# Kernel tuning notes

Hardware: AMD Instinct MI355X
Metric: run time of the kernel (lower is better)

The kernel has to match this reference:

```python
import jax, jax.numpy as jnp
import numpy as np

B, N, K, CIN, COUT = 2, 8192, 16, 64, 64


def setup_inputs() -> dict:
    key = jax.random.key(0)
    ks = jax.random.split(key, 12)
    w = lambda k, shape: jax.random.normal(k, shape, jnp.float32) * 0.02
    return dict(
        pos=jax.random.normal(ks[0], (B, N, 3), jnp.float32),
        features=jax.random.normal(ks[1], (B, N, CIN), jnp.float32),
        emb_w=w(ks[2], (CIN, COUT)), emb_b=jnp.zeros((COUT,), jnp.float32),
        wq=w(ks[3], (COUT, COUT)), wk=w(ks[4], (COUT, COUT)), wv=w(ks[5], (COUT, COUT)),
        pe_w1=w(ks[6], (3, COUT)), pe_b1=jnp.zeros((COUT,), jnp.float32),
        pe_w2=w(ks[7], (COUT, COUT)), pe_b2=jnp.zeros((COUT,), jnp.float32),
        at_w1=w(ks[8], (COUT, COUT)), at_b1=jnp.zeros((COUT,), jnp.float32),
        at_w2=w(ks[9], (COUT, COUT)), at_b2=jnp.zeros((COUT,), jnp.float32),
        out_w=w(ks[10], (COUT, CIN)), out_b=jnp.zeros((CIN,), jnp.float32),
    )


def _gather(x, idx):
    # x: [B, N, C], idx: [B, N, K] -> [B, N, K, C]
    return jax.vmap(lambda xb, ib: xb[ib])(x, idx)


def reference(pos, features, emb_w, emb_b, wq, wk, wv,
              pe_w1, pe_b1, pe_w2, pe_b2,
              at_w1, at_b1, at_w2, at_b2, out_w, out_b):
    # KNN: squared pairwise distances, take k smallest (includes self)
    sq = jnp.sum(pos * pos, axis=-1)                                  # [B, N]
    d2 = sq[:, :, None] + sq[:, None, :] - 2.0 * jnp.einsum('bnd,bmd->bnm', pos, pos)
    _, knn_idx = jax.lax.top_k(-d2, K)                                # [B, N, K]

    # recenter_groups: neighbor positions relative to query point
    grouped_pos = _gather(pos, knn_idx) - pos[:, :, None, :]          # [B, N, K, 3]

    x = features @ emb_w + emb_b                                      # [B, N, COUT]
    q = x @ wq                                                        # [B, N, COUT]
    k = _gather(x @ wk, knn_idx)                                      # [B, N, K, COUT]
    v = _gather(x @ wv, knn_idx)                                      # [B, N, K, COUT]

    # mlp_posenc: Linear(3,C) -> ReLU -> Linear(C,C)
    posenc = jax.nn.relu(grouped_pos @ pe_w1 + pe_b1) @ pe_w2 + pe_b2  # [B, N, K, COUT]

    # mlp_attn on (q - k + posenc), softmax over neighbor axis (dim=-2)
    h = q[:, :, None, :] - k + posenc
    attn = jax.nn.relu(h @ at_w1 + at_b1) @ at_w2 + at_b2
    attn = jax.nn.softmax(attn / np.float32(np.sqrt(COUT)), axis=-2)

    result = jnp.einsum('bmnf,bmnf->bmf', attn, v + posenc)           # [B, N, COUT]
    return result @ out_w + out_b + features                          # [B, N, CIN]
```

## Files before the change

kernel.cpp:

```cpp
#include <hip/hip_runtime.h>
#include <hip/hip_bf16.h>

#define BB 2
#define NN 8192
#define SPL 16
#define CAND (NN/SPL)
#define NPTS (BB*NN)

#define POS4_OFF 0u
#define PART_OFF 65536u
#define QB_OFF   4259840u
#define KVB_OFF  5308416u
#define WT_OFF   6356992u

typedef __attribute__((ext_vector_type(8))) short bf16x8;
typedef __attribute__((ext_vector_type(4))) float f32x4;

__device__ __forceinline__ unsigned umn(unsigned a, unsigned b) {
#if __has_builtin(__builtin_elementwise_min)
  return __builtin_elementwise_min(a, b);
#else
  return a < b ? a : b;
#endif
}
__device__ __forceinline__ unsigned umx(unsigned a, unsigned b) {
#if __has_builtin(__builtin_elementwise_max)
  return __builtin_elementwise_max(a, b);
#else
  return a < b ? b : a;
#endif
}

__device__ inline unsigned short f2bf(float x) {
  __hip_bfloat16 b = __float2bfloat16(x);
  return *(unsigned short*)&b;
}

#define HCOL(c, j) ((((((c) >> 3) + (j)) & 7) << 3) | ((c) & 7))

__global__ __launch_bounds__(256) void mega1(
    const float* __restrict__ pos, const float* __restrict__ feat,
    const float* __restrict__ emb_w, const float* __restrict__ emb_b,
    const float* __restrict__ wq, const float* __restrict__ wk,
    const float* __restrict__ wv,
    const float* __restrict__ pe_w2, const float* __restrict__ at_w1,
    const float* __restrict__ at_w2, const float* __restrict__ out_w,
    float* __restrict__ ws)
{
  __shared__ __align__(16) char smem[57344];
  const int tid = threadIdx.x;
  const int bx = blockIdx.x;
  float* pos4 = ws + POS4_OFF;
  unsigned* part = (unsigned*)ws + PART_OFF;
  float* qg = ws + QB_OFF;
  unsigned* kvp = (unsigned*)ws + KVB_OFF;
  unsigned short* wt = (unsigned short*)(ws + WT_OFF);

  if (bx < 512) {
    float* wl = (float*)smem;
    float* xl = (float*)(smem + 49152);
    if (tid < 32) {
      const int p = bx * 32 + tid;
      float x = pos[p * 3 + 0], y = pos[p * 3 + 1], z = pos[p * 3 + 2];
      float4 v = {x, y, z, fmaf(x, x, fmaf(y, y, z * z))};
      ((float4*)pos4)[p] = v;
    }
    for (int i = tid; i < 4096; i += 256) wl[i] = emb_w[i];
    const int col = tid & 63;
    const int rg = tid >> 6;
    const int row0 = bx * 32 + rg * 8;
    const int rowu = __builtin_amdgcn_readfirstlane(row0);
    __syncthreads();
    {
      float acc[8];
      float bias = emb_b[col];
#pragma unroll
      for (int r = 0; r < 8; r++) acc[r] = bias;
      for (int c = 0; c < 64; c++) {
        float w = wl[c * 64 + col];
        const float* fp = feat + rowu * 64 + c;
#pragma unroll
        for (int r = 0; r < 8; r++) acc[r] = fmaf(fp[r * 64], w, acc[r]);
      }
#pragma unroll
      for (int r = 0; r < 8; r++) xl[(rg * 8 + r) * 64 + col] = acc[r];
    }
    __syncthreads();
    for (int i = tid; i < 4096; i += 256) {
      wl[i] = wq[i];
      wl[4096 + i] = wk[i];
      wl[8192 + i] = wv[i];
    }
    __syncthreads();
    float aq[8], ak[8], av[8];
#pragma unroll
    for (int r = 0; r < 8; r++) { aq[r] = 0.f; ak[r] = 0.f; av[r] = 0.f; }
    for (int c = 0; c < 64; c++) {
      float w0 = wl[c * 64 + col];
      float w1 = wl[4096 + c * 64 + col];
      float w2 = wl[8192 + c * 64 + col];
#pragma unroll
      for (int r = 0; r < 8; r++) {
        float xv = xl[(rg * 8 + r) * 64 + c];
        aq[r] = fmaf(xv, w0, aq[r]);
        ak[r] = fmaf(xv, w1, ak[r]);
        av[r] = fmaf(xv, w2, av[r]);
      }
    }
#pragma unroll
    for (int r = 0; r < 8; r++) {
      qg[(row0 + r) * 64 + col] = aq[r];
      kvp[(row0 + r) * 64 + col] =
          ((unsigned)f2bf(av[r]) << 16) | (unsigned)f2bf(ak[r]);
    }
  } else if (bx < 1536) {
    constexpr int OE[63][2] = {
      {0,1},{2,3},{4,5},{6,7},{8,9},{10,11},{12,13},{14,15},
      {0,2},{1,3},{4,6},{5,7},{8,10},{9,11},{12,14},{13,15},
      {1,2},{5,6},{9,10},{13,14},
      {0,4},{1,5},{2,6},{3,7},{8,12},{9,13},{10,14},{11,15},
      {2,4},{3,5},{10,12},{11,13},
      {1,2},{3,4},{5,6},{9,10},{11,12},{13,14},
      {0,8},{1,9},{2,10},{3,11},{4,12},{5,13},{6,14},{7,15},
      {4,8},{5,9},{6,10},{7,11},
      {2,4},{3,5},{6,8},{7,9},{10,12},{11,13},
      {1,2},{3,4},{5,6},{7,8},{9,10},{11,12},{13,14}
    };
    const int vb = bx - 512;
    const int g = (vb & 63) * 256 + tid;
    const int s = vb >> 6;
    const int bu = __builtin_amdgcn_readfirstlane(g >> 13);
    const float qx = pos[g * 3 + 0], qy = pos[g * 3 + 1], qz = pos[g * 3 + 2];
    const float* __restrict__ cp = pos + (bu * NN + s * CAND) * 3;
    const unsigned jb = (unsigned)(s * CAND);
    unsigned m[16];
#pragma unroll
    for (int i = 0; i < 16; i++) m[i] = 0xFFFFFFFFu;
    for (int j0 = 0; j0 < CAND; j0 += 16) {
      float c[48];
#pragma unroll
      for (int i = 0; i < 48; i++) c[i] = cp[j0 * 3 + i];
      unsigned b[16];
#pragma unroll
      for (int i = 0; i < 16; i++) {
        float dx = c[i * 3 + 0] - qx;
        float dy = c[i * 3 + 1] - qy;
        float dz = c[i * 3 + 2] - qz;
        float d2 = fmaf(dx, dx, fmaf(dy, dy, dz * dz));
        b[i] = (__float_as_uint(d2) & 0xFFFFE000u) | (jb + (unsigned)(j0 + i));
      }
#pragma unroll
      for (int cc = 0; cc < 63; cc++) {
        const int x = OE[cc][0], y = OE[cc][1];
        unsigned lo = umn(b[x], b[y]);
        unsigned hi = umx(b[x], b[y]);
        b[x] = hi; b[y] = lo;
      }
#pragma unroll
      for (int i = 0; i < 16; i++) m[i] = umn(m[i], b[i]);
#pragma unroll
      for (int d = 8; d; d >>= 1) {
#pragma unroll
        for (int i = 0; i < 16; i++) {
          if ((i & d) == 0) {
            const int l = i | d;
            unsigned lo = umn(m[i], m[l]);
            unsigned hi = umx(m[i], m[l]);
            m[i] = lo; m[l] = hi;
          }
        }
      }
    }
#pragma unroll
    for (int i = 0; i < 16; i++)
      part[(unsigned)(s * 16 + i) * NPTS + (unsigned)g] = m[i];
  } else {
    const int t = (bx - 1536) * 256 + tid;
    const float* s;
    switch (t >> 12) {
      case 0: s = pe_w2; break;
      case 1: s = at_w1; break;
      case 2: s = at_w2; break;
      default: s = out_w; break;
    }
    const int idx = t & 4095, f = idx >> 6, c = idx & 63;
    wt[t] = f2bf(s[c * 64 + f]);
  }
}

__device__ inline void mv(const unsigned short* hm, const bf16x8 B[4][2],
                          const float bias[4], int ln, int s0, int s1,
                          f32x4 acc[4])
{
  bf16x8 a0 = *(const bf16x8*)(hm + ln * 64 + s0);
  bf16x8 a1 = *(const bf16x8*)(hm + ln * 64 + s1);
#pragma unroll
  for (int t = 0; t < 4; t++) {
    f32x4 a = {bias[t], bias[t], bias[t], bias[t]};
    a = __builtin_amdgcn_mfma_f32_16x16x32_bf16(a0, B[t][0], a, 0, 0, 0);
    a = __builtin_amdgcn_mfma_f32_16x16x32_bf16(a1, B[t][1], a, 0, 0, 0);
    acc[t] = a;
  }
}

__global__ __launch_bounds__(256, 2) void mega2(
    const float* __restrict__ ws_ro, const float* __restrict__ feat,
    const float* __restrict__ pe_w1, const float* __restrict__ pe_b1,
    const float* __restrict__ pe_b2, const float* __restrict__ at_b1,
    const float* __restrict__ at_b2, const float* __restrict__ out_b,
    float* __restrict__ out)
{
  __shared__ unsigned short hma[4][1024];
  __shared__ unsigned short resm[1024];
  __shared__ int idxm[16][16];
  const float* pos4 = ws_ro + POS4_OFF;
  const unsigned* part = (const unsigned*)ws_ro + PART_OFF;
  const float* qg = ws_ro + QB_OFF;
  const unsigned* kvp = (const unsigned*)ws_ro + KVB_OFF;
  const unsigned short* wt = (const unsigned short*)(ws_ro + WT_OFF);

  const int tid = threadIdx.x;
  const int bx = blockIdx.x;
  const int wid = tid >> 6, lane = tid & 63;
  const int ln = lane & 15, quad = lane >> 4;
  unsigned short* hm = hma[wid];
  const int s0 = ((quad + ln) & 7) << 3;
  const int s1 = ((4 + quad + ln) & 7) << 3;

  if (lane < 4) {
    const int pb = wid * 4 + lane;
    const int g = bx * 16 + pb;
    unsigned run[16];
#pragma unroll
    for (int i = 0; i < 16; i++) run[i] = part[i * NPTS + g];
#pragma unroll
    for (int l = 1; l < SPL; l++) {
#pragma unroll
      for (int i = 0; i < 16; i++)
        run[i] = umn(run[i], part[(l * 16 + 15 - i) * NPTS + g]);
#pragma unroll
      for (int d = 8; d; d >>= 1) {
#pragma unroll
        for (int i = 0; i < 16; i++) {
          if ((i & d) == 0) {
            const int l2 = i | d;
            unsigned lo = umn(run[i], run[l2]);
            unsigned hi = umx(run[i], run[l2]);
            run[i] = lo; run[l2] = hi;
          }
        }
      }
    }
    const int base = (g >> 13) * NN;
#pragma unroll
    for (int i = 0; i < 16; i++) idxm[pb][i] = base + (int)(run[i] & 0x1FFFu);
  }

  bf16x8 Bf[3][4][2];
#pragma unroll
  for (int m = 0; m < 3; m++)
#pragma unroll
    for (int t = 0; t < 4; t++)
#pragma unroll
      for (int ks = 0; ks < 2; ks++)
        Bf[m][t][ks] = *(const bf16x8*)(wt + m * 4096 + (t * 16 + ln) * 64 +
                                        ks * 32 + quad * 8);
  bf16x8 bo[2];
#pragma unroll
  for (int ks = 0; ks < 2; ks++)
    bo[ks] = *(const bf16x8*)(wt + 3 * 4096 + (wid * 16 + ln) * 64 +
                              ks * 32 + quad * 8);

  float pw10 = pe_w1[lane], pw11 = pe_w1[64 + lane], pw12 = pe_w1[128 + lane];
  float pb1 = pe_b1[lane];
  float bpe[4], ba1[4], ba2[4];
#pragma unroll
  for (int t = 0; t < 4; t++) {
    bpe[t] = pe_b2[t * 16 + ln];
    ba1[t] = at_b1[t * 16 + ln];
    ba2[t] = at_b2[t * 16 + ln];
  }
  const float4* pp4 = (const float4*)pos4;

  for (int pp = 0; pp < 4; pp++) {
    const int pb = wid * 4 + pp;
    const int p = bx * 16 + pb;
    const int ps = __builtin_amdgcn_readfirstlane(p);
    int jj[16];
#pragma unroll
    for (int u = 0; u < 4; u++) {
      int4 t4 = ((const int4*)&idxm[pb][0])[u];
      jj[u*4+0] = t4.x; jj[u*4+1] = t4.y; jj[u*4+2] = t4.z; jj[u*4+3] = t4.w;
    }
    unsigned kvw[4][4];
#pragma unroll
    for (int r = 0; r < 4; r++) {
      const unsigned* kp = kvp + jj[quad * 4 + r] * 64 + ln;
#pragma unroll
      for (int t = 0; t < 4; t++) kvw[r][t] = kp[t * 16];
    }
    float qv[4];
#pragma unroll
    for (int t = 0; t < 4; t++) qv[t] = qg[p * 64 + t * 16 + ln];

    const float4 mp = pp4[ps];
#pragma unroll
    for (int j = 0; j < 16; j++) {
      const float4 np = pp4[jj[j]];
      float h1 = fmaf(np.z - mp.z, pw12,
                 fmaf(np.y - mp.y, pw11,
                 fmaf(np.x - mp.x, pw10, pb1)));
      hm[j * 64 + HCOL(lane, j)] = f2bf(fmaxf(h1, 0.f));
    }
    f32x4 accp[4];
    mv(hm, Bf[0], bpe, ln, s0, s1, accp);
    float vpe[4][4];
#pragma unroll
    for (int r = 0; r < 4; r++) {
      const int j = quad * 4 + r;
#pragma unroll
      for (int t = 0; t < 4; t++) {
        const unsigned w = kvw[r][t];
        float kf = __uint_as_float(w << 16);
        float vf = __uint_as_float(w & 0xFFFF0000u);
        float pe = accp[t][r];
        vpe[t][r] = vf + pe;
        hm[j * 64 + HCOL(t * 16 + ln, j)] = f2bf(qv[t] - kf + pe);
      }
    }
    f32x4 acch[4];
    mv(hm, Bf[1], ba1, ln, s0, s1, acch);
#pragma unroll
    for (int t = 0; t < 4; t++)
#pragma unroll
      for (int r = 0; r < 4; r++) {
        const int j = quad * 4 + r;
        hm[j * 64 + HCOL(t * 16 + ln, j)] = f2bf(fmaxf(acch[t][r], 0.f));
      }
    f32x4 lg[4];
    mv(hm, Bf[2], ba2, ln, s0, s1, lg);
#pragma unroll
    for (int t = 0; t < 4; t++) {
      float e0 = __expf(lg[t][0] * 0.125f);
      float e1 = __expf(lg[t][1] * 0.125f);
      float e2 = __expf(lg[t][2] * 0.125f);
      float e3 = __expf(lg[t][3] * 0.125f);
      float ss = (e0 + e1) + (e2 + e3);
      float dt = fmaf(e3, vpe[t][3], fmaf(e2, vpe[t][2],
                 fmaf(e1, vpe[t][1], e0 * vpe[t][0])));
      ss += __shfl_xor(ss, 16); ss += __shfl_xor(ss, 32);
      dt += __shfl_xor(dt, 16); dt += __shfl_xor(dt, 32);
      float res = dt / ss;
      if (quad == 0) resm[pb * 64 + HCOL(t * 16 + ln, pb)] = f2bf(res);
    }
  }
  __syncthreads();
  {
    const int nt = wid;
    float ob = out_b[nt * 16 + ln];
    f32x4 acc = {ob, ob, ob, ob};
#pragma unroll
    for (int ks = 0; ks < 2; ks++) {
      bf16x8 a = *(const bf16x8*)(resm + ln * 64 +
                                  (((ks * 4 + quad + ln) & 7) << 3));
      acc = __builtin_amdgcn_mfma_f32_16x16x32_bf16(a, bo[ks], acc, 0, 0, 0);
    }
#pragma unroll
    for (int r = 0; r < 4; r++) {
      const int pt = bx * 16 + quad * 4 + r;
      const int f = nt * 16 + ln;
      out[pt * 64 + f] = acc[r] + feat[pt * 64 + f];
    }
  }
}

extern "C" void kernel_launch(void* const* d_in, const int* in_sizes, int n_in,
                              void* d_out, int out_size, void* d_ws, size_t ws_size,
                              hipStream_t stream)
{
  (void)in_sizes; (void)n_in; (void)out_size; (void)ws_size;
  const float* pos   = (const float*)d_in[0];
  const float* feat  = (const float*)d_in[1];
  const float* emb_w = (const float*)d_in[2];
  const float* emb_b = (const float*)d_in[3];
  const float* wq    = (const float*)d_in[4];
  const float* wk    = (const float*)d_in[5];
  const float* wv    = (const float*)d_in[6];
  const float* pe_w1 = (const float*)d_in[7];
  const float* pe_b1 = (const float*)d_in[8];
  const float* pe_w2 = (const float*)d_in[9];
  const float* pe_b2 = (const float*)d_in[10];
  const float* at_w1 = (const float*)d_in[11];
  const float* at_b1 = (const float*)d_in[12];
  const float* at_w2 = (const float*)d_in[13];
  const float* at_b2 = (const float*)d_in[14];
  const float* out_w = (const float*)d_in[15];
  const float* out_b = (const float*)d_in[16];
  float* ws = (float*)d_ws;

  mega1<<<1600, 256, 0, stream>>>(pos, feat, emb_w, emb_b, wq, wk, wv,
                                  pe_w2, at_w1, at_w2, out_w, ws);
  mega2<<<NPTS / 16, 256, 0, stream>>>(ws, feat, pe_w1, pe_b1, pe_b2,
                                       at_b1, at_b2, out_b, (float*)d_out);
}
```

Before: 249.7 us.

## Split into four stage kernels with precomputed pos4, dedicated KNN merge, and prefetched indices

Restructures the two mega-kernels into four launches. A small first kernel builds pos4 and the bf16 weight transposes. The second kernel runs the KNN partial search using the expanded-distance form on float4 points. Its QKV projection now loads one weight matrix at a time to shrink shared memory. A dedicated merge kernel writes the final neighbour indices to workspace, and the attention kernel prefetches the next point's indices instead of merging inside each block. This removes the serial per-block merge done by only 4 lanes per wave, at the cost of extra launches and an index round-trip through global memory. The expanded distance formula can also change neighbour selection slightly.

```diff
diff --git a/kernel.cpp b/kernel.cpp
--- a/kernel.cpp
+++ b/kernel.cpp
@@ -9,9 +9,10 @@
 
 #define POS4_OFF 0u
 #define PART_OFF 65536u
-#define QB_OFF   4259840u
-#define KVB_OFF  5308416u
-#define WT_OFF   6356992u
+#define IDX_OFF  4259840u
+#define WT_OFF   4521984u
+#define QB_OFF   4530176u
+#define KVB_OFF  5578752u
 
 typedef __attribute__((ext_vector_type(8))) short bf16x8;
 typedef __attribute__((ext_vector_type(4))) float f32x4;
@@ -38,82 +39,48 @@
 
 #define HCOL(c, j) ((((((c) >> 3) + (j)) & 7) << 3) | ((c) & 7))
 
-__global__ __launch_bounds__(256) void mega1(
-    const float* __restrict__ pos, const float* __restrict__ feat,
+__global__ __launch_bounds__(256) void s1_stage(
+    const float* __restrict__ pos,
+    const float* __restrict__ pe_w2, const float* __restrict__ at_w1,
+    const float* __restrict__ at_w2, const float* __restrict__ out_w,
+    float* __restrict__ ws)
+{
+  const int t = blockIdx.x * 256 + threadIdx.x;
+  if (t < NPTS) {
+    float x = pos[t * 3 + 0], y = pos[t * 3 + 1], z = pos[t * 3 + 2];
+    float* o = ws + POS4_OFF + t * 4;
+    o[0] = x; o[1] = y; o[2] = z;
+    o[3] = fmaf(x, x, fmaf(y, y, z * z));
+    return;
+  }
+  const int u = t - NPTS;
+  const float* s;
+  switch (u >> 12) {
+    case 0: s = pe_w2; break;
+    case 1: s = at_w1; break;
+    case 2: s = at_w2; break;
+    default: s = out_w; break;
+  }
+  const int idx = u & 4095, f = idx >> 6, c = idx & 63;
+  ((unsigned short*)(ws + WT_OFF))[u] = f2bf(s[c * 64 + f]);
+}
+
+__global__ __launch_bounds__(256) void s2_knn_qkv(
+    const float* __restrict__ feat,
     const float* __restrict__ emb_w, const float* __restrict__ emb_b,
     const float* __restrict__ wq, const float* __restrict__ wk,
     const float* __restrict__ wv,
-    const float* __restrict__ pe_w2, const float* __restrict__ at_w1,
-    const float* __restrict__ at_w2, const float* __restrict__ out_w,
     float* __restrict__ ws)
 {
-  __shared__ __align__(16) char smem[57344];
+  __shared__ __align__(16) float smem[6144];
   const int tid = threadIdx.x;
   const int bx = blockIdx.x;
-  float* pos4 = ws + POS4_OFF;
+  const float* pos4 = ws + POS4_OFF;
   unsigned* part = (unsigned*)ws + PART_OFF;
   float* qg = ws + QB_OFF;
   unsigned* kvp = (unsigned*)ws + KVB_OFF;
-  unsigned short* wt = (unsigned short*)(ws + WT_OFF);
-
-  if (bx < 512) {
-    float* wl = (float*)smem;
-    float* xl = (float*)(smem + 49152);
-    if (tid < 32) {
-      const int p = bx * 32 + tid;
-      float x = pos[p * 3 + 0], y = pos[p * 3 + 1], z = pos[p * 3 + 2];
-      float4 v = {x, y, z, fmaf(x, x, fmaf(y, y, z * z))};
-      ((float4*)pos4)[p] = v;
-    }
-    for (int i = tid; i < 4096; i += 256) wl[i] = emb_w[i];
-    const int col = tid & 63;
-    const int rg = tid >> 6;
-    const int row0 = bx * 32 + rg * 8;
-    const int rowu = __builtin_amdgcn_readfirstlane(row0);
-    __syncthreads();
-    {
-      float acc[8];
-      float bias = emb_b[col];
-#pragma unroll
-      for (int r = 0; r < 8; r++) acc[r] = bias;
-      for (int c = 0; c < 64; c++) {
-        float w = wl[c * 64 + col];
-        const float* fp = feat + rowu * 64 + c;
-#pragma unroll
-        for (int r = 0; r < 8; r++) acc[r] = fmaf(fp[r * 64], w, acc[r]);
-      }
-#pragma unroll
-      for (int r = 0; r < 8; r++) xl[(rg * 8 + r) * 64 + col] = acc[r];
-    }
-    __syncthreads();
-    for (int i = tid; i < 4096; i += 256) {
-      wl[i] = wq[i];
-      wl[4096 + i] = wk[i];
-      wl[8192 + i] = wv[i];
-    }
-    __syncthreads();
-    float aq[8], ak[8], av[8];
-#pragma unroll
-    for (int r = 0; r < 8; r++) { aq[r] = 0.f; ak[r] = 0.f; av[r] = 0.f; }
-    for (int c = 0; c < 64; c++) {
-      float w0 = wl[c * 64 + col];
-      float w1 = wl[4096 + c * 64 + col];
-      float w2 = wl[8192 + c * 64 + col];
-#pragma unroll
-      for (int r = 0; r < 8; r++) {
-        float xv = xl[(rg * 8 + r) * 64 + c];
-        aq[r] = fmaf(xv, w0, aq[r]);
-        ak[r] = fmaf(xv, w1, ak[r]);
-        av[r] = fmaf(xv, w2, av[r]);
-      }
-    }
-#pragma unroll
-    for (int r = 0; r < 8; r++) {
-      qg[(row0 + r) * 64 + col] = aq[r];
-      kvp[(row0 + r) * 64 + col] =
-          ((unsigned)f2bf(av[r]) << 16) | (unsigned)f2bf(ak[r]);
-    }
-  } else if (bx < 1536) {
+
+  if (bx < 1024) {
     constexpr int OE[63][2] = {
       {0,1},{2,3},{4,5},{6,7},{8,9},{10,11},{12,13},{14,15},
       {0,2},{1,3},{4,6},{5,7},{8,10},{9,11},{12,14},{13,15},
@@ -126,27 +93,24 @@
       {2,4},{3,5},{6,8},{7,9},{10,12},{11,13},
       {1,2},{3,4},{5,6},{7,8},{9,10},{11,12},{13,14}
     };
-    const int vb = bx - 512;
-    const int g = (vb & 63) * 256 + tid;
-    const int s = vb >> 6;
+    const int g = (bx & 63) * 256 + tid;
+    const int s = bx >> 6;
     const int bu = __builtin_amdgcn_readfirstlane(g >> 13);
-    const float qx = pos[g * 3 + 0], qy = pos[g * 3 + 1], qz = pos[g * 3 + 2];
-    const float* __restrict__ cp = pos + (bu * NN + s * CAND) * 3;
+    const float4* allp = (const float4*)pos4;
+    const float4 q = allp[g];
+    const float qx2 = -2.f * q.x, qy2 = -2.f * q.y, qz2 = -2.f * q.z;
+    const float sqq = q.w + 1e-5f;
+    const float4* cand = allp + (bu * NN + s * CAND);
     const unsigned jb = (unsigned)(s * CAND);
     unsigned m[16];
 #pragma unroll
     for (int i = 0; i < 16; i++) m[i] = 0xFFFFFFFFu;
     for (int j0 = 0; j0 < CAND; j0 += 16) {
-      float c[48];
-#pragma unroll
-      for (int i = 0; i < 48; i++) c[i] = cp[j0 * 3 + i];
       unsigned b[16];
 #pragma unroll
       for (int i = 0; i < 16; i++) {
-        float dx = c[i * 3 + 0] - qx;
-        float dy = c[i * 3 + 1] - qy;
-        float dz = c[i * 3 + 2] - qz;
-        float d2 = fmaf(dx, dx, fmaf(dy, dy, dz * dz));
+        float4 cp = cand[j0 + i];
+        float d2 = fmaf(cp.x, qx2, fmaf(cp.y, qy2, fmaf(cp.z, qz2, cp.w + sqq)));
         b[i] = (__float_as_uint(d2) & 0xFFFFE000u) | (jb + (unsigned)(j0 + i));
       }
 #pragma unroll
@@ -175,17 +139,115 @@
     for (int i = 0; i < 16; i++)
       part[(unsigned)(s * 16 + i) * NPTS + (unsigned)g] = m[i];
   } else {
-    const int t = (bx - 1536) * 256 + tid;
-    const float* s;
-    switch (t >> 12) {
-      case 0: s = pe_w2; break;
-      case 1: s = at_w1; break;
-      case 2: s = at_w2; break;
-      default: s = out_w; break;
-    }
-    const int idx = t & 4095, f = idx >> 6, c = idx & 63;
-    wt[t] = f2bf(s[c * 64 + f]);
-  }
+    float* wl = smem;
+    float* xl = smem + 4096;
+    const int vb = bx - 1024;
+    const int col = tid & 63;
+    const int rg = tid >> 6;
+    const int row0 = vb * 32 + rg * 8;
+    const int rowu = __builtin_amdgcn_readfirstlane(row0);
+    for (int i = tid; i < 4096; i += 256) wl[i] = emb_w[i];
+    __syncthreads();
+    {
+      float acc[8];
+      float bias = emb_b[col];
+#pragma unroll
+      for (int r = 0; r < 8; r++) acc[r] = bias;
+      for (int c = 0; c < 64; c++) {
+        float w = wl[c * 64 + col];
+        const float* fp = feat + rowu * 64 + c;
+#pragma unroll
+        for (int r = 0; r < 8; r++) acc[r] = fmaf(fp[r * 64], w, acc[r]);
+      }
+#pragma unroll
+      for (int r = 0; r < 8; r++) xl[(rg * 8 + r) * 64 + col] = acc[r];
+    }
+    __syncthreads();
+    for (int i = tid; i < 4096; i += 256) wl[i] = wq[i];
+    __syncthreads();
+    {
+      float aq[8];
+#pragma unroll
+      for (int r = 0; r < 8; r++) aq[r] = 0.f;
+      for (int c = 0; c < 64; c++) {
+        float w = wl[c * 64 + col];
+#pragma unroll
+        for (int r = 0; r < 8; r++)
+          aq[r] = fmaf(xl[(rg * 8 + r) * 64 + c], w, aq[r]);
+      }
+#pragma unroll
+      for (int r = 0; r < 8; r++) qg[(row0 + r) * 64 + col] = aq[r];
+    }
+    __syncthreads();
+    for (int i = tid; i < 4096; i += 256) wl[i] = wk[i];
+    __syncthreads();
+    float ak[8];
+    {
+#pragma unroll
+      for (int r = 0; r < 8; r++) ak[r] = 0.f;
+      for (int c = 0; c < 64; c++) {
+        float w = wl[c * 64 + col];
+#pragma unroll
+        for (int r = 0; r < 8; r++)
+          ak[r] = fmaf(xl[(rg * 8 + r) * 64 + c], w, ak[r]);
+      }
+    }
+    __syncthreads();
+    for (int i = tid; i < 4096; i += 256) wl[i] = wv[i];
+    __syncthreads();
+    {
+      float av[8];
+#pragma unroll
+      for (int r = 0; r < 8; r++) av[r] = 0.f;
+      for (int c = 0; c < 64; c++) {
+        float w = wl[c * 64 + col];
+#pragma unroll
+        for (int r = 0; r < 8; r++)
+          av[r] = fmaf(xl[(rg * 8 + r) * 64 + c], w, av[r]);
+      }
+#pragma unroll
+      for (int r = 0; r < 8; r++)
+        kvp[(row0 + r) * 64 + col] =
+            ((unsigned)f2bf(av[r]) << 16) | (unsigned)f2bf(ak[r]);
+    }
+  }
+}
+
+__global__ __launch_bounds__(256) void s3_merge(const float* __restrict__ ws_ro,
+                                                int* __restrict__ knn_idx)
+{
+  const unsigned* part = (const unsigned*)ws_ro + PART_OFF;
+  const int g = blockIdx.x * 256 + threadIdx.x;
+  unsigned run[16];
+#pragma unroll
+  for (int i = 0; i < 16; i++) run[i] = part[i * NPTS + g];
+#pragma unroll
+  for (int l = 1; l < SPL; l++) {
+#pragma unroll
+    for (int i = 0; i < 16; i++)
+      run[i] = umn(run[i], part[(l * 16 + 15 - i) * NPTS + g]);
+#pragma unroll
+    for (int d = 8; d; d >>= 1) {
+#pragma unroll
+      for (int i = 0; i < 16; i++) {
+        if ((i & d) == 0) {
+          const int l2 = i | d;
+          unsigned lo = umn(run[i], run[l2]);
+          unsigned hi = umx(run[i], run[l2]);
+          run[i] = lo; run[l2] = hi;
+        }
+      }
+    }
+  }
+  const int base = (g >> 13) * NN;
+  int outv[16];
+#pragma unroll
+  for (int i = 0; i < 16; i++) outv[i] = base + (int)(run[i] & 0x1FFFu);
+  int4* o = (int4*)(knn_idx + g * 16);
+  o[0] = make_int4(outv[0], outv[1], outv[2], outv[3]);
+  o[1] = make_int4(outv[4], outv[5], outv[6], outv[7]);
+  o[2] = make_int4(outv[8], outv[9], outv[10], outv[11]);
+  o[3] = make_int4(outv[12], outv[13], outv[14], outv[15]);
 }
 
 __device__ inline void mv(const unsigned short* hm, const bf16x8 B[4][2],
@@ -203,59 +265,27 @@
   }
 }
 
-__global__ __launch_bounds__(256, 2) void mega2(
+__global__ __launch_bounds__(256, 2) void s4_attn(
     const float* __restrict__ ws_ro, const float* __restrict__ feat,
     const float* __restrict__ pe_w1, const float* __restrict__ pe_b1,
     const float* __restrict__ pe_b2, const float* __restrict__ at_b1,
     const float* __restrict__ at_b2, const float* __restrict__ out_b,
-    float* __restrict__ out)
+    const int* __restrict__ knn, float* __restrict__ out)
 {
   __shared__ unsigned short hma[4][1024];
   __shared__ unsigned short resm[1024];
-  __shared__ int idxm[16][16];
   const float* pos4 = ws_ro + POS4_OFF;
-  const unsigned* part = (const unsigned*)ws_ro + PART_OFF;
   const float* qg = ws_ro + QB_OFF;
   const unsigned* kvp = (const unsigned*)ws_ro + KVB_OFF;
   const unsigned short* wt = (const unsigned short*)(ws_ro + WT_OFF);
 
   const int tid = threadIdx.x;
-  const int bx = blockIdx.x;
   const int wid = tid >> 6, lane = tid & 63;
   const int ln = lane & 15, quad = lane >> 4;
   unsigned short* hm = hma[wid];
   const int s0 = ((quad + ln) & 7) << 3;
   const int s1 = ((4 + quad + ln) & 7) << 3;
 
-  if (lane < 4) {
-    const int pb = wid * 4 + lane;
-    const int g = bx * 16 + pb;
-    unsigned run[16];
-#pragma unroll
-    for (int i = 0; i < 16; i++) run[i] = part[i * NPTS + g];
-#pragma unroll
-    for (int l = 1; l < SPL; l++) {
-#pragma unroll
-      for (int i = 0; i < 16; i++)
-        run[i] = umn(run[i], part[(l * 16 + 15 - i) * NPTS + g]);
-#pragma unroll
-      for (int d = 8; d; d >>= 1) {
-#pragma unroll
-        for (int i = 0; i < 16; i++) {
-          if ((i & d) == 0) {
-            const int l2 = i | d;
-            unsigned lo = umn(run[i], run[l2]);
-            unsigned hi = umx(run[i], run[l2]);
-            run[i] = lo; run[l2] = hi;
-          }
-        }
-      }
-    }
-    const int base = (g >> 13) * NN;
-#pragma unroll
-    for (int i = 0; i < 16; i++) idxm[pb][i] = base + (int)(run[i] & 0x1FFFu);
-  }
-
   bf16x8 Bf[3][4][2];
 #pragma unroll
   for (int m = 0; m < 3; m++)
@@ -282,15 +312,30 @@
   }
   const float4* pp4 = (const float4*)pos4;
 
+  const int p0 = blockIdx.x * 16 + wid * 4;
+  const int ps0 = __builtin_amdgcn_readfirstlane(p0);
+  int4 cur[4];
+  {
+    const int4* ip4 = (const int4*)(knn + ps0 * 16);
+#pragma unroll
+    for (int u = 0; u < 4; u++) cur[u] = ip4[u];
+  }
+
   for (int pp = 0; pp < 4; pp++) {
-    const int pb = wid * 4 + pp;
-    const int p = bx * 16 + pb;
+    const int p = p0 + pp;
     const int ps = __builtin_amdgcn_readfirstlane(p);
     int jj[16];
 #pragma unroll
     for (int u = 0; u < 4; u++) {
-      int4 t4 = ((const int4*)&idxm[pb][0])[u];
-      jj[u*4+0] = t4.x; jj[u*4+1] = t4.y; jj[u*4+2] = t4.z; jj[u*4+3] = t4.w;
+      jj[u*4+0] = cur[u].x; jj[u*4+1] = cur[u].y;
+      jj[u*4+2] = cur[u].z; jj[u*4+3] = cur[u].w;
+    }
+    int4 nxt[4];
+    {
+      const int pn = (pp < 3) ? (ps + 1) : ps;
+      const int4* np4 = (const int4*)(knn + pn * 16);
+#pragma unroll
+      for (int u = 0; u < 4; u++) nxt[u] = np4[u];
     }
     unsigned kvw[4][4];
 #pragma unroll
@@ -339,6 +384,7 @@
       }
     f32x4 lg[4];
     mv(hm, Bf[2], ba2, ln, s0, s1, lg);
+    const int pb = wid * 4 + pp;
 #pragma unroll
     for (int t = 0; t < 4; t++) {
       float e0 = __expf(lg[t][0] * 0.125f);
@@ -353,6 +399,8 @@
       float res = dt / ss;
       if (quad == 0) resm[pb * 64 + HCOL(t * 16 + ln, pb)] = f2bf(res);
     }
+#pragma unroll
+    for (int u = 0; u < 4; u++) cur[u] = nxt[u];
   }
   __syncthreads();
   {
@@ -367,7 +415,7 @@
     }
 #pragma unroll
     for (int r = 0; r < 4; r++) {
-      const int pt = bx * 16 + quad * 4 + r;
+      const int pt = blockIdx.x * 16 + quad * 4 + r;
       const int f = nt * 16 + ln;
       out[pt * 64 + f] = acc[r] + feat[pt * 64 + f];
     }
@@ -398,8 +446,9 @@
   const float* out_b = (const float*)d_in[16];
   float* ws = (float*)d_ws;
 
-  mega1<<<1600, 256, 0, stream>>>(pos, feat, emb_w, emb_b, wq, wk, wv,
-                                  pe_w2, at_w1, at_w2, out_w, ws);
-  mega2<<<NPTS / 16, 256, 0, stream>>>(ws, feat, pe_w1, pe_b1, pe_b2,
-                                       at_b1, at_b2, out_b, (float*)d_out);
-}
+  s1_stage<<<128, 256, 0, stream>>>(pos, pe_w2, at_w1, at_w2, out_w, ws);
+  s2_knn_qkv<<<1536, 256, 0, stream>>>(feat, emb_w, emb_b, wq, wk, wv, ws);
+  s3_merge<<<64, 256, 0, stream>>>(ws, (int*)ws + IDX_OFF);
+  s4_attn<<<NPTS / 16, 256, 0, stream>>>(ws, feat, pe_w1, pe_b1, pe_b2,
+      at_b1, at_b2, out_b, (int*)ws + IDX_OFF, (float*)d_out);
+}
```

Measured after the change: 228.4 us. 1.09x faster.
